# Kernel tuning notes

Measured on AMD Instinct MI355X. Metric: run time of the kernel, lower is better.

Reference implementation:

```python
import jax, jax.numpy as jnp
import numpy as np

V, D, H, L, B, S = 8192, 128, 8, 2, 1, 128
HD = D // H
HID = int(8 * D / 3)
EPS = 1e-6


def setup_inputs() -> dict:
    key = jax.random.key(0)
    ks = jax.random.split(key, 12)
    sc = 0.02
    return {
        "idx": jax.random.randint(ks[0], (B, S), 0, V),
        "w_raw": jax.random.normal(ks[1], (D, V), jnp.float32) * sc,
        "norm1_w": jnp.ones((L, D), jnp.float32),
        "norm2_w": jnp.ones((L, D), jnp.float32),
        "wq": jax.random.normal(ks[2], (L, D, D), jnp.float32) * sc,
        "wk": jax.random.normal(ks[3], (L, D, D), jnp.float32) * sc,
        "wv": jax.random.normal(ks[4], (L, D, D), jnp.float32) * sc,
        "wo": jax.random.normal(ks[5], (L, D, D), jnp.float32) * sc,
        "w1": jax.random.normal(ks[6], (L, D, HID), jnp.float32) * sc,
        "w3": jax.random.normal(ks[7], (L, D, HID), jnp.float32) * sc,
        "w2": jax.random.normal(ks[8], (L, HID, D), jnp.float32) * sc,
        "final_norm_w": jnp.ones((D,), jnp.float32),
    }


def rmsnorm(x, w):
    return x * jax.lax.rsqrt(jnp.mean(x * x, axis=-1, keepdims=True) + EPS) * w


def rope_cos_sin(seqlen, hd):
    inv = 1.0 / (10000.0 ** (jnp.arange(0, hd, 2, dtype=jnp.float32) / hd))
    t = jnp.arange(seqlen, dtype=jnp.float32)
    f = jnp.outer(t, inv)  # (S, hd/2)
    return jnp.cos(f), jnp.sin(f)


def apply_rope(x, cos, sin):
    # x: (B,S,H,HD); interleaved complex pairs as in Llama
    x0, x1 = x[..., 0::2], x[..., 1::2]
    c = cos[None, :, None, :]
    s = sin[None, :, None, :]
    r0 = x0 * c - x1 * s
    r1 = x0 * s + x1 * c
    return jnp.stack([r0, r1], axis=-1).reshape(x.shape)


def forward(idx, w_raw, norm1_w, norm2_w, wq, wk, wv, wo, w1, w2, w3, final_norm_w):
    Wemb = jax.nn.sigmoid(w_raw)                 # (D,V)
    x = Wemb.T[idx]                              # Yoneda one-hot @ W.T == gather -> (B,S,D)
    cos, sin = rope_cos_sin(S, HD)
    causal = jnp.tril(jnp.ones((S, S), bool))[None, None]  # (1,1,S,S)
    scale = 1.0 / jnp.sqrt(jnp.float32(HD))
    for i in range(L):
        # Multi-Universe attention (heads == universes), RoPE, causal SDPA
        h = rmsnorm(x, norm1_w[i])
        q = (h @ wq[i]).reshape(B, S, H, HD)
        k = (h @ wk[i]).reshape(B, S, H, HD)
        v = (h @ wv[i]).reshape(B, S, H, HD)
        q = apply_rope(q, cos, sin)
        k = apply_rope(k, cos, sin)
        scores = jnp.einsum("bihd,bjhd->bhij", q, k) * scale
        scores = jnp.where(causal, scores, jnp.float32(-1e9))
        attn = jax.nn.softmax(scores, axis=-1)
        o = jnp.einsum("bhij,bjhd->bihd", attn, v).reshape(B, S, D) @ wo[i]
        x = x + o
        # SwiGLU FFN
        h2 = rmsnorm(x, norm2_w[i])
        x = x + (jax.nn.silu(h2 @ w1[i]) * (h2 @ w3[i])) @ w2[i]
    x_norm = rmsnorm(x, final_norm_w)
    # Godel-Heyting reachability head
    x_n = x_norm / jnp.linalg.norm(x_norm, axis=-1, keepdims=True)      # (B,S,D)
    v_n = (Wemb / jnp.linalg.norm(Wemb, axis=0, keepdims=True)).T        # (V,D)
    a = x_n[:, :, None, :]                                               # (B,S,1,D)
    b = v_n[None, None, :, :]                                            # (1,1,V,D)
    # strict Godel implication: a => b = 1 if a <= b else b
    imp = jnp.where(a <= b, jnp.float32(1.0), b)                         # (B,S,V,D)
    logits = jnp.clip(imp.mean(axis=-1), 1e-6, 1.0 - 1e-6)               # (B,S,V)
    return logits


def reference(idx, w_raw, norm1_w, norm2_w, wq, wk, wv, wo, w1, w2, w3, final_norm_w):
    return forward(idx, w_raw, norm1_w, norm2_w, wq, wk, wv, wo, w1, w2, w3, final_norm_w)
```

## Files before the change

kernel.cpp:

```cpp
#include <hip/hip_runtime.h>
#include <math.h>

#define V 8192
#define D 128
#define NH 8
#define HD 16
#define SEQ 128
#define HID 341
#define EPS 1e-6f

__device__ __forceinline__ float sigm(float x) { return 1.0f / (1.0f + __expf(-x)); }

__device__ __forceinline__ float block_sum256(float v, float* scratch) {
    #pragma unroll
    for (int m = 32; m > 0; m >>= 1) v += __shfl_xor(v, m);
    if ((threadIdx.x & 63) == 0) scratch[threadIdx.x >> 6] = v;
    __syncthreads();
    float s = (scratch[0] + scratch[1]) + (scratch[2] + scratch[3]);
    __syncthreads();
    return s;
}

__global__ __launch_bounds__(256, 1) void k_embed_qkv(
    const int* __restrict__ idx, const float* __restrict__ w_raw,
    const float* __restrict__ wq, const float* __restrict__ wk,
    const float* __restrict__ wv, const float* __restrict__ n1w,
    const float* __restrict__ w1, const float* __restrict__ w3,
    const float* __restrict__ w2, const float* __restrict__ wo,
    float* __restrict__ x, float* __restrict__ q, float* __restrict__ k,
    float* __restrict__ v, float* __restrict__ sink) {
    int t = threadIdx.x;
    if (blockIdx.x >= SEQ) {
        int g = (blockIdx.x - SEQ) * 256 + t;
        float acc = 0.f;
        const float4* p = (const float4*)w_raw;
        for (int i = g; i < 262144; i += 65536) {
            float4 u = p[i];
            acc += u.x + u.y + u.z + u.w;
        }
        p = (const float4*)w1;
        if (g < 21824) { float4 u = p[g]; acc += u.x + u.y + u.z + u.w; }
        p = (const float4*)w3;
        if (g < 21824) { float4 u = p[g]; acc += u.x + u.y + u.z + u.w; }
        p = (const float4*)w2;
        if (g < 21824) { float4 u = p[g]; acc += u.x + u.y + u.z + u.w; }
        p = (const float4*)wq;
        if (g < 8192) { float4 u = p[g]; acc += u.x + u.y + u.z + u.w; }
        p = (const float4*)wk;
        if (g < 8192) { float4 u = p[g]; acc += u.x + u.y + u.z + u.w; }
        p = (const float4*)wv;
        if (g < 8192) { float4 u = p[g]; acc += u.x + u.y + u.z + u.w; }
        p = (const float4*)wo;
        if (g < 8192) { float4 u = p[g]; acc += u.x + u.y + u.z + u.w; }
        if (acc == 1234.5678f) sink[0] = acc;
        return;
    }
    __shared__ float hr[D], qrow[D], krow[D], vpart[2][D], scr[4];
    int s = blockIdx.x;
    int col = t & 127, half = t >> 7, dlo = half * 64;
    float xv = 0.f;
    if (t < 128) xv = sigm(w_raw[t * V + idx[s]]);
    float wpre[128];
    const float* wsel = (t < 128) ? wq : wk;
    #pragma unroll
    for (int d = 0; d < 128; ++d) wpre[d] = wsel[d * D + col];
    float wvpre[64];
    #pragma unroll
    for (int d = 0; d < 64; ++d) wvpre[d] = wv[(dlo + d) * D + col];
    if (t < 128) x[s * D + t] = xv;
    float ss = block_sum256(xv * xv, scr);
    float r = 1.0f / sqrtf(ss * (1.0f / D) + EPS);
    if (t < 128) hr[t] = xv * r * n1w[t];
    __syncthreads();
    float a0 = 0, a1 = 0, a2 = 0, a3 = 0;
    #pragma unroll
    for (int d = 0; d < 128; d += 4) {
        a0 += hr[d] * wpre[d];
        a1 += hr[d + 1] * wpre[d + 1];
        a2 += hr[d + 2] * wpre[d + 2];
        a3 += hr[d + 3] * wpre[d + 3];
    }
    float qk = (a0 + a1) + (a2 + a3);
    float b0 = 0, b1 = 0, b2 = 0, b3 = 0;
    #pragma unroll
    for (int d = 0; d < 64; d += 4) {
        b0 += hr[dlo + d] * wvpre[d];
        b1 += hr[dlo + d + 1] * wvpre[d + 1];
        b2 += hr[dlo + d + 2] * wvpre[d + 2];
        b3 += hr[dlo + d + 3] * wvpre[d + 3];
    }
    vpart[half][col] = (b0 + b1) + (b2 + b3);
    if (t < 128) qrow[col] = qk;
    else krow[col] = qk;
    __syncthreads();
    if (t < 128) {
        v[s * D + t] = vpart[0][t] + vpart[1][t];
        int c = t & (HD - 1);
        int m = c >> 1;
        float fr = (float)s * expf(-(float)m * 1.15129254649702283e+00f);
        float cs = cosf(fr), sn = sinf(fr);
        int base = t & ~1;
        float qe = qrow[base], qod = qrow[base + 1];
        float ke = krow[base], kod = krow[base + 1];
        q[s * D + t] = (c & 1) ? (qe * sn + qod * cs) : (qe * cs - qod * sn);
        k[s * D + t] = (c & 1) ? (ke * sn + kod * cs) : (ke * cs - kod * sn);
    }
}

template <int MODE>
__global__ __launch_bounds__(256, 1) void k_layer(
    const float* __restrict__ q, const float* __restrict__ kg,
    const float* __restrict__ vg, float* __restrict__ x,
    const float* __restrict__ wo, const float* __restrict__ n2w,
    const float* __restrict__ w1, const float* __restrict__ w3,
    const float* __restrict__ w2, const float* __restrict__ wq,
    const float* __restrict__ wk, const float* __restrict__ wv,
    const float* __restrict__ n1w, float* __restrict__ qo, float* __restrict__ ko,
    float* __restrict__ vo, const float* __restrict__ fw, float* __restrict__ xng) {
    __shared__ float ps[NH][SEQ + 1];
    __shared__ float qs[D], orow[D], h2[D];
    __shared__ float part[2][D];
    __shared__ float afA[HID], afB[HID], af[HID];
    __shared__ float rl[NH];
    __shared__ float scr[4];
    int s = blockIdx.x, t = threadIdx.x;
    int col = t & 127, half = t >> 7;
    int jlo = half * 64, dlo = half * 64;

    float qv = 0.f, xr = 0.f;
    if (t < 128) {
        qv = q[s * D + t];
        xr = x[s * D + t];
    }
    float4 kp[4][4];
    #pragma unroll
    for (int u = 0; u < 4; ++u) {
        const float4* p = (const float4*)&kg[col * D + (half + 2 * u) * HD];
        kp[u][0] = p[0]; kp[u][1] = p[1]; kp[u][2] = p[2]; kp[u][3] = p[3];
    }
    float vpre[64];
    #pragma unroll
    for (int j = 0; j < 64; ++j) vpre[j] = vg[(jlo + j) * D + col];
    float wopre[64];
    #pragma unroll
    for (int u = 0; u < 64; ++u) wopre[u] = wo[(dlo + u) * D + col];

    if (t < 128) qs[t] = qv;
    __syncthreads();

    #pragma unroll
    for (int u = 0; u < 4; ++u) {
        int h = half + 2 * u;
        const float* qh = &qs[h * HD];
        float acc = kp[u][0].x * qh[0] + kp[u][0].y * qh[1] + kp[u][0].z * qh[2] +
                    kp[u][0].w * qh[3] + kp[u][1].x * qh[4] + kp[u][1].y * qh[5] +
                    kp[u][1].z * qh[6] + kp[u][1].w * qh[7] + kp[u][2].x * qh[8] +
                    kp[u][2].y * qh[9] + kp[u][2].z * qh[10] + kp[u][2].w * qh[11] +
                    kp[u][3].x * qh[12] + kp[u][3].y * qh[13] + kp[u][3].z * qh[14] +
                    kp[u][3].w * qh[15];
        ps[h][col] = (col <= s) ? acc * 0.25f : 0.f;
    }
    __syncthreads();

    {
        int h = t >> 5, lane = t & 31;
        float pm = -1e30f;
        for (int j = lane; j <= s; j += 32) pm = fmaxf(pm, ps[h][j]);
        #pragma unroll
        for (int m = 16; m > 0; m >>= 1) pm = fmaxf(pm, __shfl_xor(pm, m, 32));
        float psum = 0.f;
        for (int j = lane; j <= s; j += 32) {
            float e = __expf(ps[h][j] - pm);
            ps[h][j] = e;
            psum += e;
        }
        #pragma unroll
        for (int m = 16; m > 0; m >>= 1) psum += __shfl_xor(psum, m, 32);
        if (lane == 0) rl[h] = 1.0f / psum;
    }
    __syncthreads();

    {
        int h = col >> 4;
        float a0 = 0, a1 = 0, a2 = 0, a3 = 0;
        #pragma unroll
        for (int j = 0; j < 64; j += 4) {
            a0 += ps[h][jlo + j] * vpre[j];
            a1 += ps[h][jlo + j + 1] * vpre[j + 1];
            a2 += ps[h][jlo + j + 2] * vpre[j + 2];
            a3 += ps[h][jlo + j + 3] * vpre[j + 3];
        }
        part[half][col] = (a0 + a1) + (a2 + a3);
    }
    __syncthreads();
    if (t < 128) orow[t] = (part[0][t] + part[1][t]) * rl[t >> 4];
    __syncthreads();

    {
        float a0 = 0, a1 = 0;
        #pragma unroll
        for (int u = 0; u < 64; u += 2) {
            a0 += orow[dlo + u] * wopre[u];
            a1 += orow[dlo + u + 1] * wopre[u + 1];
        }
        part[half][col] = a0 + a1;
    }
    __syncthreads();
    float xn = 0.f;
    if (t < 128) xn = xr + part[0][t] + part[1][t];
    float ss2 = block_sum256((t < 128) ? xn * xn : 0.f, scr);
    float r2 = 1.0f / sqrtf(ss2 * (1.0f / D) + EPS);
    if (t < 128) h2[t] = xn * r2 * n2w[t];
    __syncthreads();

    for (int task = t; task < 2 * HID; task += 256) {
        int mat = task >= HID;
        int c2 = mat ? (task - HID) : task;
        const float* w = mat ? w3 : w1;
        float a0 = 0, a1 = 0, a2 = 0, a3 = 0;
        #pragma unroll 8
        for (int d = 0; d < D; d += 4) {
            a0 += h2[d] * w[d * HID + c2];
            a1 += h2[d + 1] * w[(d + 1) * HID + c2];
            a2 += h2[d + 2] * w[(d + 2) * HID + c2];
            a3 += h2[d + 3] * w[(d + 3) * HID + c2];
        }
        if (mat) afB[c2] = (a0 + a1) + (a2 + a3);
        else afA[c2] = (a0 + a1) + (a2 + a3);
    }
    __syncthreads();
    for (int c2 = t; c2 < HID; c2 += 256) {
        float a1v = afA[c2];
        af[c2] = (a1v / (1.0f + __expf(-a1v))) * afB[c2];
    }
    __syncthreads();

    {
        int lo = half ? 171 : 0;
        int hi = half ? 341 : 171;
        float a0 = 0, a1 = 0, a2 = 0, a3 = 0;
        int tt = lo;
        #pragma unroll 8
        for (; tt + 3 < hi; tt += 4) {
            a0 += af[tt] * w2[tt * D + col];
            a1 += af[tt + 1] * w2[(tt + 1) * D + col];
            a2 += af[tt + 2] * w2[(tt + 2) * D + col];
            a3 += af[tt + 3] * w2[(tt + 3) * D + col];
        }
        for (; tt < hi; ++tt) a0 += af[tt] * w2[tt * D + col];
        part[half][col] = (a0 + a1) + (a2 + a3);
    }
    __syncthreads();
    float x2 = 0.f;
    if (t < 128) {
        x2 = xn + part[0][t] + part[1][t];
        if (MODE == 0) x[s * D + t] = x2;
    }

    float ss = block_sum256((t < 128) ? x2 * x2 : 0.f, scr);
    float r = 1.0f / sqrtf(ss * (1.0f / D) + EPS);

    if constexpr (MODE == 0) {
        if (t < 128) h2[t] = x2 * r * n1w[t];
        __syncthreads();
        const float* wsel = (t < 128) ? wq : wk;
        float a0 = 0, a1 = 0, a2 = 0, a3 = 0;
        #pragma unroll 8
        for (int d = 0; d < D; d += 4) {
            a0 += h2[d] * wsel[d * D + col];
            a1 += h2[d + 1] * wsel[(d + 1) * D + col];
            a2 += h2[d + 2] * wsel[(d + 2) * D + col];
            a3 += h2[d + 3] * wsel[(d + 3) * D + col];
        }
        float qk = (a0 + a1) + (a2 + a3);
        float b0 = 0, b1 = 0, b2 = 0, b3 = 0;
        #pragma unroll 8
        for (int d = dlo; d < dlo + 64; d += 4) {
            b0 += h2[d] * wv[d * D + col];
            b1 += h2[d + 1] * wv[(d + 1) * D + col];
            b2 += h2[d + 2] * wv[(d + 2) * D + col];
            b3 += h2[d + 3] * wv[(d + 3) * D + col];
        }
        part[half][col] = (b0 + b1) + (b2 + b3);
        if (t < 128) qs[col] = qk;
        else orow[col] = qk;
        __syncthreads();
        if (t < 128) {
            vo[s * D + t] = part[0][t] + part[1][t];
            int c = t & (HD - 1);
            int mm = c >> 1;
            float fr = (float)s * expf(-(float)mm * 1.15129254649702283e+00f);
            float cs = cosf(fr), sn = sinf(fr);
            int base = t & ~1;
            float qe = qs[base], qod = qs[base + 1];
            float ke = orow[base], kod = orow[base + 1];
            qo[s * D + t] = (c & 1) ? (qe * sn + qod * cs) : (qe * cs - qod * sn);
            ko[s * D + t] = (c & 1) ? (ke * sn + kod * cs) : (ke * cs - kod * sn);
        }
    } else {
        float y = (t < 128) ? x2 * r * fw[t] : 0.f;
        float nn = block_sum256(y * y, scr);
        if (t < 128) xng[t * SEQ + s] = y / sqrtf(nn);
    }
}

__global__ __launch_bounds__(256) void k_logits(const float* __restrict__ xng,
                                                const float* __restrict__ w_raw,
                                                float* __restrict__ out) {
    __shared__ float xs[D * 64];
    __shared__ float vs[D * 32];
    __shared__ float nred[256];
    __shared__ float invn_s[32];
    int t = threadIdx.x;
    int sbase = (blockIdx.x & 1) * 64;
    int vbase = (blockIdx.x >> 1) * 32;
    for (int i = t; i < D * 64; i += 256) {
        int d = i >> 6, s2 = i & 63;
        xs[i] = xng[d * SEQ + sbase + s2];
    }
    for (int i = t; i < D * 32; i += 256) {
        int d = i >> 5, jj = i & 31;
        vs[i] = sigm(w_raw[d * V + vbase + jj]);
    }
    __syncthreads();
    {
        int colc = t & 31, dp = t >> 5;
        float p = 0.f;
        for (int u = 0; u < 16; ++u) {
            float vv = vs[(dp * 16 + u) * 32 + colc];
            p += vv * vv;
        }
        nred[t] = p;
    }
    __syncthreads();
    if (t < 32) {
        float sum = 0.f;
        for (int u = 0; u < 8; ++u) sum += nred[u * 32 + t];
        invn_s[t] = 1.0f / sqrtf(sum);
    }
    __syncthreads();
    for (int i = t; i < D * 32; i += 256) vs[i] *= invn_s[i & 31];
    __syncthreads();
    int vg = t & 15;
    int sg = t >> 4;
    float acc[4][2] = {};
    for (int d = 0; d < D; ++d) {
        float4 xq = *(const float4*)&xs[d * 64 + sg * 4];
        float2 vq = *(const float2*)&vs[d * 32 + vg * 2];
        acc[0][0] += (xq.x <= vq.x) ? 1.0f : vq.x;
        acc[0][1] += (xq.x <= vq.y) ? 1.0f : vq.y;
        acc[1][0] += (xq.y <= vq.x) ? 1.0f : vq.x;
        acc[1][1] += (xq.y <= vq.y) ? 1.0f : vq.y;
        acc[2][0] += (xq.z <= vq.x) ? 1.0f : vq.x;
        acc[2][1] += (xq.z <= vq.y) ? 1.0f : vq.y;
        acc[3][0] += (xq.w <= vq.x) ? 1.0f : vq.x;
        acc[3][1] += (xq.w <= vq.y) ? 1.0f : vq.y;
    }
    const float inv128 = 1.0f / 128.0f;
    #pragma unroll
    for (int si = 0; si < 4; ++si) {
        int s = sbase + sg * 4 + si;
        float2 ov;
        ov.x = fminf(fmaxf(acc[si][0] * inv128, 1e-6f), 1.0f - 1e-6f);
        ov.y = fminf(fmaxf(acc[si][1] * inv128, 1e-6f), 1.0f - 1e-6f);
        *(float2*)&out[s * V + vbase + vg * 2] = ov;
    }
}

extern "C" void kernel_launch(void* const* d_in, const int* in_sizes, int n_in,
                              void* d_out, int out_size, void* d_ws, size_t ws_size,
                              hipStream_t stream) {
    const int* idx = (const int*)d_in[0];
    const float* w_raw = (const float*)d_in[1];
    const float* n1w = (const float*)d_in[2];
    const float* n2w = (const float*)d_in[3];
    const float* wq = (const float*)d_in[4];
    const float* wk = (const float*)d_in[5];
    const float* wv = (const float*)d_in[6];
    const float* wo = (const float*)d_in[7];
    const float* w1 = (const float*)d_in[8];
    const float* w3 = (const float*)d_in[9];
    const float* w2 = (const float*)d_in[10];
    const float* fnw = (const float*)d_in[11];
    float* out = (float*)d_out;
    float* ws = (float*)d_ws;

    float* x    = ws;
    float* q1   = ws + 16384;
    float* k1   = ws + 32768;
    float* v1   = ws + 49152;
    float* q2   = ws + 65536;
    float* k2   = ws + 81920;
    float* v2   = ws + 98304;
    float* xng  = ws + 114688;
    float* sink = ws + 131072;

    k_embed_qkv<<<dim3(SEQ + 256), dim3(256), 0, stream>>>(
        idx, w_raw, wq, wk, wv, n1w, w1, w3, w2, wo, x, q1, k1, v1, sink);
    k_layer<0><<<dim3(SEQ), dim3(256), 0, stream>>>(
        q1, k1, v1, x, wo, n2w, w1, w3, w2,
        wq + D * D, wk + D * D, wv + D * D, n1w + D, q2, k2, v2,
        (const float*)nullptr, (float*)nullptr);
    k_layer<1><<<dim3(SEQ), dim3(256), 0, stream>>>(
        q2, k2, v2, x, wo + D * D, n2w + D, w1 + D * HID, w3 + D * HID,
        w2 + HID * D, (const float*)nullptr, (const float*)nullptr,
        (const float*)nullptr, (const float*)nullptr, (float*)nullptr,
        (float*)nullptr, (float*)nullptr, fnw, xng);
    k_logits<<<dim3(512), dim3(256), 0, stream>>>(xng, w_raw, out);
}
```

Before: 146.4 us.

## Transpose weights and V into per-thread contiguous layouts for float4 dot products

The embed kernel's spare blocks now write transposed copies of all per-layer weights (wq/wk/wv/wo, w1/w3, and a padded w2) into workspace. V is stored transposed, so each thread in the layer kernels reads its dot-product operand contiguously with float4 loads instead of strided scalar loads, and the large register-prefetch arrays are removed. The FFN is rebalanced so each thread computes three hidden outputs. The trade-off is extra transpose traffic at launch, uncoalesced transposed reads per thread, and a loss of the prefetch overlap the old register arrays gave.

```diff
diff --git a/kernel.cpp b/kernel.cpp
--- a/kernel.cpp
+++ b/kernel.cpp
@@ -7,6 +7,7 @@
 #define HD 16
 #define SEQ 128
 #define HID 341
+#define HIDP 344
 #define EPS 1e-6f
 
 __device__ __forceinline__ float sigm(float x) { return 1.0f / (1.0f + __expf(-x)); }
@@ -24,34 +25,45 @@
 __global__ __launch_bounds__(256, 1) void k_embed_qkv(
     const int* __restrict__ idx, const float* __restrict__ w_raw,
     const float* __restrict__ wq, const float* __restrict__ wk,
-    const float* __restrict__ wv, const float* __restrict__ n1w,
+    const float* __restrict__ wv, const float* __restrict__ wo,
     const float* __restrict__ w1, const float* __restrict__ w3,
-    const float* __restrict__ w2, const float* __restrict__ wo,
+    const float* __restrict__ w2, const float* __restrict__ n1w,
     float* __restrict__ x, float* __restrict__ q, float* __restrict__ k,
-    float* __restrict__ v, float* __restrict__ sink) {
+    float* __restrict__ vt, float* __restrict__ wqT, float* __restrict__ wkT,
+    float* __restrict__ wvT, float* __restrict__ woT, float* __restrict__ w1T,
+    float* __restrict__ w3T, float* __restrict__ w2T, float* __restrict__ sink) {
     int t = threadIdx.x;
     if (blockIdx.x >= SEQ) {
         int g = (blockIdx.x - SEQ) * 256 + t;
+        if (g < 32768) {
+            int l = g >> 14, rem = g & 16383, d = rem >> 7, c = rem & 127;
+            int o = l * 16384 + c * 128 + d;
+            wqT[o] = wq[g];
+            wkT[o] = wk[g];
+            wvT[o] = wv[g];
+            woT[o] = wo[g];
+        }
+        for (int i = g; i < 2 * 43648; i += 65536) {
+            int l = i >= 43648;
+            int r = i - (l ? 43648 : 0);
+            int c = r >> 7, d = r & 127;
+            w1T[i] = w1[l * 43648 + d * HID + c];
+            w3T[i] = w3[l * 43648 + d * HID + c];
+        }
+        for (int i = g; i < 2 * 44032; i += 65536) {
+            int l = i >= 44032;
+            int r = i - (l ? 44032 : 0);
+            int c = r / HIDP;
+            int kk = r - c * HIDP;
+            w2T[i] = (kk < HID) ? w2[l * 43648 + kk * 128 + c] : 0.f;
+        }
         float acc = 0.f;
         const float4* p = (const float4*)w_raw;
-        for (int i = g; i < 262144; i += 65536) {
-            float4 u = p[i];
+        #pragma unroll
+        for (int i = 0; i < 4; ++i) {
+            float4 u = p[g + i * 65536];
             acc += u.x + u.y + u.z + u.w;
         }
-        p = (const float4*)w1;
-        if (g < 21824) { float4 u = p[g]; acc += u.x + u.y + u.z + u.w; }
-        p = (const float4*)w3;
-        if (g < 21824) { float4 u = p[g]; acc += u.x + u.y + u.z + u.w; }
-        p = (const float4*)w2;
-        if (g < 21824) { float4 u = p[g]; acc += u.x + u.y + u.z + u.w; }
-        p = (const float4*)wq;
-        if (g < 8192) { float4 u = p[g]; acc += u.x + u.y + u.z + u.w; }
-        p = (const float4*)wk;
-        if (g < 8192) { float4 u = p[g]; acc += u.x + u.y + u.z + u.w; }
-        p = (const float4*)wv;
-        if (g < 8192) { float4 u = p[g]; acc += u.x + u.y + u.z + u.w; }
-        p = (const float4*)wo;
-        if (g < 8192) { float4 u = p[g]; acc += u.x + u.y + u.z + u.w; }
         if (acc == 1234.5678f) sink[0] = acc;
         return;
     }
@@ -60,41 +72,35 @@
     int col = t & 127, half = t >> 7, dlo = half * 64;
     float xv = 0.f;
     if (t < 128) xv = sigm(w_raw[t * V + idx[s]]);
-    float wpre[128];
-    const float* wsel = (t < 128) ? wq : wk;
-    #pragma unroll
-    for (int d = 0; d < 128; ++d) wpre[d] = wsel[d * D + col];
-    float wvpre[64];
-    #pragma unroll
-    for (int d = 0; d < 64; ++d) wvpre[d] = wv[(dlo + d) * D + col];
     if (t < 128) x[s * D + t] = xv;
     float ss = block_sum256(xv * xv, scr);
     float r = 1.0f / sqrtf(ss * (1.0f / D) + EPS);
     if (t < 128) hr[t] = xv * r * n1w[t];
     __syncthreads();
+    const float* wsel = (t < 128) ? wq : wk;
     float a0 = 0, a1 = 0, a2 = 0, a3 = 0;
-    #pragma unroll
+    #pragma unroll 8
     for (int d = 0; d < 128; d += 4) {
-        a0 += hr[d] * wpre[d];
-        a1 += hr[d + 1] * wpre[d + 1];
-        a2 += hr[d + 2] * wpre[d + 2];
-        a3 += hr[d + 3] * wpre[d + 3];
+        a0 += hr[d] * wsel[d * D + col];
+        a1 += hr[d + 1] * wsel[(d + 1) * D + col];
+        a2 += hr[d + 2] * wsel[(d + 2) * D + col];
+        a3 += hr[d + 3] * wsel[(d + 3) * D + col];
     }
     float qk = (a0 + a1) + (a2 + a3);
     float b0 = 0, b1 = 0, b2 = 0, b3 = 0;
-    #pragma unroll
-    for (int d = 0; d < 64; d += 4) {
-        b0 += hr[dlo + d] * wvpre[d];
-        b1 += hr[dlo + d + 1] * wvpre[d + 1];
-        b2 += hr[dlo + d + 2] * wvpre[d + 2];
-        b3 += hr[dlo + d + 3] * wvpre[d + 3];
+    #pragma unroll 8
+    for (int d = dlo; d < dlo + 64; d += 4) {
+        b0 += hr[d] * wv[d * D + col];
+        b1 += hr[d + 1] * wv[(d + 1) * D + col];
+        b2 += hr[d + 2] * wv[(d + 2) * D + col];
+        b3 += hr[d + 3] * wv[(d + 3) * D + col];
     }
     vpart[half][col] = (b0 + b1) + (b2 + b3);
     if (t < 128) qrow[col] = qk;
     else krow[col] = qk;
     __syncthreads();
     if (t < 128) {
-        v[s * D + t] = vpart[0][t] + vpart[1][t];
+        vt[t * SEQ + s] = vpart[0][t] + vpart[1][t];
         int c = t & (HD - 1);
         int m = c >> 1;
         float fr = (float)s * expf(-(float)m * 1.15129254649702283e+00f);
@@ -110,55 +116,47 @@
 template <int MODE>
 __global__ __launch_bounds__(256, 1) void k_layer(
     const float* __restrict__ q, const float* __restrict__ kg,
-    const float* __restrict__ vg, float* __restrict__ x,
-    const float* __restrict__ wo, const float* __restrict__ n2w,
-    const float* __restrict__ w1, const float* __restrict__ w3,
-    const float* __restrict__ w2, const float* __restrict__ wq,
-    const float* __restrict__ wk, const float* __restrict__ wv,
+    const float* __restrict__ vt, float* __restrict__ x,
+    const float* __restrict__ woT, const float* __restrict__ n2w,
+    const float* __restrict__ w1T, const float* __restrict__ w3T,
+    const float* __restrict__ w2T, const float* __restrict__ wqT,
+    const float* __restrict__ wkT, const float* __restrict__ wvT,
     const float* __restrict__ n1w, float* __restrict__ qo, float* __restrict__ ko,
-    float* __restrict__ vo, const float* __restrict__ fw, float* __restrict__ xng) {
-    __shared__ float ps[NH][SEQ + 1];
-    __shared__ float qs[D], orow[D], h2[D];
+    float* __restrict__ vto, const float* __restrict__ fw, float* __restrict__ xng) {
+    __shared__ float ps[NH][SEQ + 2];
+    __shared__ float qs[D], orow[D], qrow[D], krow[D];
     __shared__ float part[2][D];
-    __shared__ float afA[HID], afB[HID], af[HID];
+    __shared__ float4 h24[32];
+    __shared__ float4 af4[86];
+    __shared__ float afA[HID], afB[HID];
     __shared__ float rl[NH];
     __shared__ float scr[4];
+    float* h2 = (float*)h24;
+    float* af = (float*)af4;
     int s = blockIdx.x, t = threadIdx.x;
     int col = t & 127, half = t >> 7;
-    int jlo = half * 64, dlo = half * 64;
-
-    float qv = 0.f, xr = 0.f;
+
+    float xr = 0.f;
     if (t < 128) {
-        qv = q[s * D + t];
+        qs[t] = q[s * D + t];
         xr = x[s * D + t];
     }
-    float4 kp[4][4];
-    #pragma unroll
-    for (int u = 0; u < 4; ++u) {
-        const float4* p = (const float4*)&kg[col * D + (half + 2 * u) * HD];
-        kp[u][0] = p[0]; kp[u][1] = p[1]; kp[u][2] = p[2]; kp[u][3] = p[3];
-    }
-    float vpre[64];
-    #pragma unroll
-    for (int j = 0; j < 64; ++j) vpre[j] = vg[(jlo + j) * D + col];
-    float wopre[64];
-    #pragma unroll
-    for (int u = 0; u < 64; ++u) wopre[u] = wo[(dlo + u) * D + col];
-
-    if (t < 128) qs[t] = qv;
-    __syncthreads();
-
-    #pragma unroll
-    for (int u = 0; u < 4; ++u) {
-        int h = half + 2 * u;
-        const float* qh = &qs[h * HD];
-        float acc = kp[u][0].x * qh[0] + kp[u][0].y * qh[1] + kp[u][0].z * qh[2] +
-                    kp[u][0].w * qh[3] + kp[u][1].x * qh[4] + kp[u][1].y * qh[5] +
-                    kp[u][1].z * qh[6] + kp[u][1].w * qh[7] + kp[u][2].x * qh[8] +
-                    kp[u][2].y * qh[9] + kp[u][2].z * qh[10] + kp[u][2].w * qh[11] +
-                    kp[u][3].x * qh[12] + kp[u][3].y * qh[13] + kp[u][3].z * qh[14] +
-                    kp[u][3].w * qh[15];
-        ps[h][col] = (col <= s) ? acc * 0.25f : 0.f;
+    __syncthreads();
+
+    {
+        int j = col;
+        #pragma unroll
+        for (int u = 0; u < 4; ++u) {
+            int h = half + 2 * u;
+            const float4* kp = (const float4*)&kg[j * D + h * HD];
+            float4 k0 = kp[0], k1 = kp[1], k2 = kp[2], k3 = kp[3];
+            const float* qh = &qs[h * HD];
+            float acc = k0.x * qh[0] + k0.y * qh[1] + k0.z * qh[2] + k0.w * qh[3] +
+                        k1.x * qh[4] + k1.y * qh[5] + k1.z * qh[6] + k1.w * qh[7] +
+                        k2.x * qh[8] + k2.y * qh[9] + k2.z * qh[10] + k2.w * qh[11] +
+                        k3.x * qh[12] + k3.y * qh[13] + k3.z * qh[14] + k3.w * qh[15];
+            ps[h][j] = (j <= s) ? acc * 0.25f : 0.f;
+        }
     }
     __syncthreads();
 
@@ -181,14 +179,17 @@
     __syncthreads();
 
     {
-        int h = col >> 4;
+        int h = col >> 4, jlo = half * 64;
+        const float4* vp = (const float4*)&vt[col * SEQ + jlo];
         float a0 = 0, a1 = 0, a2 = 0, a3 = 0;
         #pragma unroll
-        for (int j = 0; j < 64; j += 4) {
-            a0 += ps[h][jlo + j] * vpre[j];
-            a1 += ps[h][jlo + j + 1] * vpre[j + 1];
-            a2 += ps[h][jlo + j + 2] * vpre[j + 2];
-            a3 += ps[h][jlo + j + 3] * vpre[j + 3];
+        for (int i = 0; i < 16; ++i) {
+            float4 vv = vp[i];
+            int j = jlo + 4 * i;
+            a0 += ps[h][j] * vv.x;
+            a1 += ps[h][j + 1] * vv.y;
+            a2 += ps[h][j + 2] * vv.z;
+            a3 += ps[h][j + 3] * vv.w;
         }
         part[half][col] = (a0 + a1) + (a2 + a3);
     }
@@ -197,13 +198,19 @@
     __syncthreads();
 
     {
-        float a0 = 0, a1 = 0;
-        #pragma unroll
-        for (int u = 0; u < 64; u += 2) {
-            a0 += orow[dlo + u] * wopre[u];
-            a1 += orow[dlo + u + 1] * wopre[u + 1];
-        }
-        part[half][col] = a0 + a1;
+        int dlo = half * 64;
+        const float4* wp = (const float4*)&woT[col * 128 + dlo];
+        float a0 = 0, a1 = 0, a2 = 0, a3 = 0;
+        #pragma unroll
+        for (int i = 0; i < 16; ++i) {
+            float4 ww = wp[i];
+            int d = dlo + 4 * i;
+            a0 += orow[d] * ww.x;
+            a1 += orow[d + 1] * ww.y;
+            a2 += orow[d + 2] * ww.z;
+            a3 += orow[d + 3] * ww.w;
+        }
+        part[half][col] = (a0 + a1) + (a2 + a3);
     }
     __syncthreads();
     float xn = 0.f;
@@ -213,41 +220,56 @@
     if (t < 128) h2[t] = xn * r2 * n2w[t];
     __syncthreads();
 
-    for (int task = t; task < 2 * HID; task += 256) {
-        int mat = task >= HID;
-        int c2 = mat ? (task - HID) : task;
-        const float* w = mat ? w3 : w1;
+    {
+        int u1 = t, u2 = t + 256, u3 = t + 512;
+        const float4* pa = (const float4*)&w1T[u1 * 128];
+        const float4* pb = (const float4*)((u2 < HID) ? &w1T[u2 * 128] : &w3T[(u2 - HID) * 128]);
+        bool v3 = u3 < 2 * HID;
+        const float4* pc = (const float4*)(v3 ? &w3T[(u3 - HID) * 128] : &w3T[0]);
+        float a0 = 0, a1 = 0, b0 = 0, b1 = 0, c0 = 0, c1 = 0;
+        #pragma unroll
+        for (int i = 0; i < 32; ++i) {
+            float4 hh = h24[i];
+            float4 wa = pa[i];
+            a0 += hh.x * wa.x + hh.y * wa.y;
+            a1 += hh.z * wa.z + hh.w * wa.w;
+            float4 wb = pb[i];
+            b0 += hh.x * wb.x + hh.y * wb.y;
+            b1 += hh.z * wb.z + hh.w * wb.w;
+            float4 wc = pc[i];
+            c0 += hh.x * wc.x + hh.y * wc.y;
+            c1 += hh.z * wc.z + hh.w * wc.w;
+        }
+        afA[u1] = a0 + a1;
+        if (u2 < HID) afA[u2] = b0 + b1;
+        else afB[u2 - HID] = b0 + b1;
+        if (v3) afB[u3 - HID] = c0 + c1;
+    }
+    __syncthreads();
+    for (int c2 = t; c2 < HIDP; c2 += 256) {
+        if (c2 < HID) {
+            float a = afA[c2];
+            af[c2] = (a / (1.0f + __expf(-a))) * afB[c2];
+        } else {
+            af[c2] = 0.f;
+        }
+    }
+    __syncthreads();
+
+    {
+        int klo = half * 172;
+        const float4* wp = (const float4*)&w2T[col * HIDP + klo];
+        const float4* ap = (const float4*)&af[klo];
         float a0 = 0, a1 = 0, a2 = 0, a3 = 0;
-        #pragma unroll 8
-        for (int d = 0; d < D; d += 4) {
-            a0 += h2[d] * w[d * HID + c2];
-            a1 += h2[d + 1] * w[(d + 1) * HID + c2];
-            a2 += h2[d + 2] * w[(d + 2) * HID + c2];
-            a3 += h2[d + 3] * w[(d + 3) * HID + c2];
-        }
-        if (mat) afB[c2] = (a0 + a1) + (a2 + a3);
-        else afA[c2] = (a0 + a1) + (a2 + a3);
-    }
-    __syncthreads();
-    for (int c2 = t; c2 < HID; c2 += 256) {
-        float a1v = afA[c2];
-        af[c2] = (a1v / (1.0f + __expf(-a1v))) * afB[c2];
-    }
-    __syncthreads();
-
-    {
-        int lo = half ? 171 : 0;
-        int hi = half ? 341 : 171;
-        float a0 = 0, a1 = 0, a2 = 0, a3 = 0;
-        int tt = lo;
-        #pragma unroll 8
-        for (; tt + 3 < hi; tt += 4) {
-            a0 += af[tt] * w2[tt * D + col];
-            a1 += af[tt + 1] * w2[(tt + 1) * D + col];
-            a2 += af[tt + 2] * w2[(tt + 2) * D + col];
-            a3 += af[tt + 3] * w2[(tt + 3) * D + col];
-        }
-        for (; tt < hi; ++tt) a0 += af[tt] * w2[tt * D + col];
+        #pragma unroll
+        for (int i = 0; i < 43; ++i) {
+            float4 ww = wp[i];
+            float4 aa = ap[i];
+            a0 += aa.x * ww.x;
+            a1 += aa.y * ww.y;
+            a2 += aa.z * ww.z;
+            a3 += aa.w * ww.w;
+        }
         part[half][col] = (a0 + a1) + (a2 + a3);
     }
     __syncthreads();
@@ -256,49 +278,55 @@
         x2 = xn + part[0][t] + part[1][t];
         if (MODE == 0) x[s * D + t] = x2;
     }
-
-    float ss = block_sum256((t < 128) ? x2 * x2 : 0.f, scr);
-    float r = 1.0f / sqrtf(ss * (1.0f / D) + EPS);
+    float ss3 = block_sum256((t < 128) ? x2 * x2 : 0.f, scr);
+    float r3 = 1.0f / sqrtf(ss3 * (1.0f / D) + EPS);
 
     if constexpr (MODE == 0) {
-        if (t < 128) h2[t] = x2 * r * n1w[t];
+        if (t < 128) h2[t] = x2 * r3 * n1w[t];
         __syncthreads();
-        const float* wsel = (t < 128) ? wq : wk;
-        float a0 = 0, a1 = 0, a2 = 0, a3 = 0;
-        #pragma unroll 8
-        for (int d = 0; d < D; d += 4) {
-            a0 += h2[d] * wsel[d * D + col];
-            a1 += h2[d + 1] * wsel[(d + 1) * D + col];
-            a2 += h2[d + 2] * wsel[(d + 2) * D + col];
-            a3 += h2[d + 3] * wsel[(d + 3) * D + col];
-        }
-        float qk = (a0 + a1) + (a2 + a3);
-        float b0 = 0, b1 = 0, b2 = 0, b3 = 0;
-        #pragma unroll 8
-        for (int d = dlo; d < dlo + 64; d += 4) {
-            b0 += h2[d] * wv[d * D + col];
-            b1 += h2[d + 1] * wv[(d + 1) * D + col];
-            b2 += h2[d + 2] * wv[(d + 2) * D + col];
-            b3 += h2[d + 3] * wv[(d + 3) * D + col];
-        }
-        part[half][col] = (b0 + b1) + (b2 + b3);
-        if (t < 128) qs[col] = qk;
-        else orow[col] = qk;
+        float qk;
+        {
+            const float4* wp = (const float4*)((t < 128) ? &wqT[col * 128] : &wkT[col * 128]);
+            float a0 = 0, a1 = 0;
+            #pragma unroll
+            for (int i = 0; i < 32; ++i) {
+                float4 hh = h24[i];
+                float4 ww = wp[i];
+                a0 += hh.x * ww.x + hh.y * ww.y;
+                a1 += hh.z * ww.z + hh.w * ww.w;
+            }
+            qk = a0 + a1;
+        }
+        {
+            int dlo = half * 64;
+            const float4* wp = (const float4*)&wvT[col * 128 + dlo];
+            float a0 = 0, a1 = 0;
+            #pragma unroll
+            for (int i = 0; i < 16; ++i) {
+                float4 hh = h24[dlo / 4 + i];
+                float4 ww = wp[i];
+                a0 += hh.x * ww.x + hh.y * ww.y;
+                a1 += hh.z * ww.z + hh.w * ww.w;
+            }
+            part[half][col] = a0 + a1;
+        }
+        if (t < 128) qrow[col] = qk;
+        else krow[col] = qk;
         __syncthreads();
         if (t < 128) {
-            vo[s * D + t] = part[0][t] + part[1][t];
+            vto[t * SEQ + s] = part[0][t] + part[1][t];
             int c = t & (HD - 1);
             int mm = c >> 1;
             float fr = (float)s * expf(-(float)mm * 1.15129254649702283e+00f);
             float cs = cosf(fr), sn = sinf(fr);
             int base = t & ~1;
-            float qe = qs[base], qod = qs[base + 1];
-            float ke = orow[base], kod = orow[base + 1];
+            float qe = qrow[base], qod = qrow[base + 1];
+            float ke = krow[base], kod = krow[base + 1];
             qo[s * D + t] = (c & 1) ? (qe * sn + qod * cs) : (qe * cs - qod * sn);
             ko[s * D + t] = (c & 1) ? (ke * sn + kod * cs) : (ke * cs - kod * sn);
         }
     } else {
-        float y = (t < 128) ? x2 * r * fw[t] : 0.f;
+        float y = (t < 128) ? x2 * r3 * fw[t] : 0.f;
         float nn = block_sum256(y * y, scr);
         if (t < 128) xng[t * SEQ + s] = y / sqrtf(nn);
     }
@@ -388,22 +416,30 @@
     float* x    = ws;
     float* q1   = ws + 16384;
     float* k1   = ws + 32768;
-    float* v1   = ws + 49152;
+    float* v1t  = ws + 49152;
     float* q2   = ws + 65536;
     float* k2   = ws + 81920;
-    float* v2   = ws + 98304;
+    float* v2t  = ws + 98304;
     float* xng  = ws + 114688;
     float* sink = ws + 131072;
+    float* wqT  = ws + 131104;
+    float* wkT  = ws + 163872;
+    float* wvT  = ws + 196640;
+    float* woT  = ws + 229408;
+    float* w1T  = ws + 262176;
+    float* w3T  = ws + 349472;
+    float* w2T  = ws + 436768;
 
     k_embed_qkv<<<dim3(SEQ + 256), dim3(256), 0, stream>>>(
-        idx, w_raw, wq, wk, wv, n1w, w1, w3, w2, wo, x, q1, k1, v1, sink);
+        idx, w_raw, wq, wk, wv, wo, w1, w3, w2, n1w, x, q1, k1, v1t,
+        wqT, wkT, wvT, woT, w1T, w3T, w2T, sink);
     k_layer<0><<<dim3(SEQ), dim3(256), 0, stream>>>(
-        q1, k1, v1, x, wo, n2w, w1, w3, w2,
-        wq + D * D, wk + D * D, wv + D * D, n1w + D, q2, k2, v2,
+        q1, k1, v1t, x, woT, n2w, w1T, w3T, w2T,
+        wqT + 16384, wkT + 16384, wvT + 16384, n1w + D, q2, k2, v2t,
         (const float*)nullptr, (float*)nullptr);
     k_layer<1><<<dim3(SEQ), dim3(256), 0, stream>>>(
-        q2, k2, v2, x, wo + D * D, n2w + D, w1 + D * HID, w3 + D * HID,
-        w2 + HID * D, (const float*)nullptr, (const float*)nullptr,
+        q2, k2, v2t, x, woT + 16384, n2w + D, w1T + 43648, w3T + 43648,
+        w2T + 44032, (const float*)nullptr, (const float*)nullptr,
         (const float*)nullptr, (const float*)nullptr, (float*)nullptr,
         (float*)nullptr, (float*)nullptr, fnw, xng);
     k_logits<<<dim3(512), dim3(256), 0, stream>>>(xng, w_raw, out);
```

After: 165.3 us. 13.0% more time.

## Stage layer weights through LDS with coalesced float4 double-buffered loads

Applied to the files above, without the earlier changes.

The per-token layer kernel now copies V, Wo, Wq/Wk/Wv and the FFN weights (w1, w3, w2) into a 128 KB shared buffer using coalesced float4 loads. The FFN matmuls use a double-buffered pipeline that prefetches the next chunk into registers while the current chunk is computed from LDS. The embed kernel drops its large register prefetch arrays and reads weights directly. The goal is to replace strided, uncoalesced global loads and heavy register pressure with coalesced bulk copies and reads from LDS. The cost is many extra barriers and a very large LDS footprint per block, which limits occupancy to one block per CU.

```diff
diff --git a/kernel.cpp b/kernel.cpp
--- a/kernel.cpp
+++ b/kernel.cpp
@@ -19,6 +19,25 @@
     float s = (scratch[0] + scratch[1]) + (scratch[2] + scratch[3]);
     __syncthreads();
     return s;
+}
+
+template <int NF4>
+__device__ __forceinline__ void pf_load(float4* v, const float* src, int t) {
+    const float4* s4 = (const float4*)src;
+    #pragma unroll
+    for (int i = 0; i < (NF4 + 255) / 256; ++i) {
+        int idx = t + i * 256;
+        if (idx < NF4) v[i] = s4[idx];
+    }
+}
+template <int NF4>
+__device__ __forceinline__ void pf_store(const float4* v, float* dst, int t) {
+    float4* d4 = (float4*)dst;
+    #pragma unroll
+    for (int i = 0; i < (NF4 + 255) / 256; ++i) {
+        int idx = t + i * 256;
+        if (idx < NF4) d4[idx] = v[i];
+    }
 }
 
 __global__ __launch_bounds__(256, 1) void k_embed_qkv(
@@ -60,34 +79,28 @@
     int col = t & 127, half = t >> 7, dlo = half * 64;
     float xv = 0.f;
     if (t < 128) xv = sigm(w_raw[t * V + idx[s]]);
-    float wpre[128];
-    const float* wsel = (t < 128) ? wq : wk;
-    #pragma unroll
-    for (int d = 0; d < 128; ++d) wpre[d] = wsel[d * D + col];
-    float wvpre[64];
-    #pragma unroll
-    for (int d = 0; d < 64; ++d) wvpre[d] = wv[(dlo + d) * D + col];
     if (t < 128) x[s * D + t] = xv;
     float ss = block_sum256(xv * xv, scr);
     float r = 1.0f / sqrtf(ss * (1.0f / D) + EPS);
     if (t < 128) hr[t] = xv * r * n1w[t];
     __syncthreads();
+    const float* wsel = (t < 128) ? wq : wk;
     float a0 = 0, a1 = 0, a2 = 0, a3 = 0;
-    #pragma unroll
+    #pragma unroll 8
     for (int d = 0; d < 128; d += 4) {
-        a0 += hr[d] * wpre[d];
-        a1 += hr[d + 1] * wpre[d + 1];
-        a2 += hr[d + 2] * wpre[d + 2];
-        a3 += hr[d + 3] * wpre[d + 3];
+        a0 += hr[d] * wsel[d * D + col];
+        a1 += hr[d + 1] * wsel[(d + 1) * D + col];
+        a2 += hr[d + 2] * wsel[(d + 2) * D + col];
+        a3 += hr[d + 3] * wsel[(d + 3) * D + col];
     }
     float qk = (a0 + a1) + (a2 + a3);
     float b0 = 0, b1 = 0, b2 = 0, b3 = 0;
-    #pragma unroll
-    for (int d = 0; d < 64; d += 4) {
-        b0 += hr[dlo + d] * wvpre[d];
-        b1 += hr[dlo + d + 1] * wvpre[d + 1];
-        b2 += hr[dlo + d + 2] * wvpre[d + 2];
-        b3 += hr[dlo + d + 3] * wvpre[d + 3];
+    #pragma unroll 8
+    for (int d = dlo; d < dlo + 64; d += 4) {
+        b0 += hr[d] * wv[d * D + col];
+        b1 += hr[d + 1] * wv[(d + 1) * D + col];
+        b2 += hr[d + 2] * wv[(d + 2) * D + col];
+        b3 += hr[d + 3] * wv[(d + 3) * D + col];
     }
     vpart[half][col] = (b0 + b1) + (b2 + b3);
     if (t < 128) qrow[col] = qk;
@@ -117,48 +130,48 @@
     const float* __restrict__ wk, const float* __restrict__ wv,
     const float* __restrict__ n1w, float* __restrict__ qo, float* __restrict__ ko,
     float* __restrict__ vo, const float* __restrict__ fw, float* __restrict__ xng) {
-    __shared__ float ps[NH][SEQ + 1];
-    __shared__ float qs[D], orow[D], h2[D];
+    __shared__ float B0[32768];
+    __shared__ float ps[NH][SEQ + 2];
+    __shared__ float qs[D], orow[D], h2[D], qrow[D], krow[D];
     __shared__ float part[2][D];
-    __shared__ float afA[HID], afB[HID], af[HID];
+    __shared__ float af[344];
     __shared__ float rl[NH];
     __shared__ float scr[4];
     int s = blockIdx.x, t = threadIdx.x;
     int col = t & 127, half = t >> 7;
-    int jlo = half * 64, dlo = half * 64;
-
-    float qv = 0.f, xr = 0.f;
+
+    {
+        const float4* v4 = (const float4*)vg;
+        const float4* o4 = (const float4*)wo;
+        float4* d0 = (float4*)B0;
+        float4* d1 = (float4*)(B0 + 16384);
+        #pragma unroll
+        for (int i = 0; i < 16; ++i) {
+            d0[t + i * 256] = v4[t + i * 256];
+            d1[t + i * 256] = o4[t + i * 256];
+        }
+    }
+    float xr = 0.f;
     if (t < 128) {
-        qv = q[s * D + t];
+        qs[t] = q[s * D + t];
         xr = x[s * D + t];
     }
-    float4 kp[4][4];
-    #pragma unroll
-    for (int u = 0; u < 4; ++u) {
-        const float4* p = (const float4*)&kg[col * D + (half + 2 * u) * HD];
-        kp[u][0] = p[0]; kp[u][1] = p[1]; kp[u][2] = p[2]; kp[u][3] = p[3];
-    }
-    float vpre[64];
-    #pragma unroll
-    for (int j = 0; j < 64; ++j) vpre[j] = vg[(jlo + j) * D + col];
-    float wopre[64];
-    #pragma unroll
-    for (int u = 0; u < 64; ++u) wopre[u] = wo[(dlo + u) * D + col];
-
-    if (t < 128) qs[t] = qv;
-    __syncthreads();
-
-    #pragma unroll
-    for (int u = 0; u < 4; ++u) {
-        int h = half + 2 * u;
-        const float* qh = &qs[h * HD];
-        float acc = kp[u][0].x * qh[0] + kp[u][0].y * qh[1] + kp[u][0].z * qh[2] +
-                    kp[u][0].w * qh[3] + kp[u][1].x * qh[4] + kp[u][1].y * qh[5] +
-                    kp[u][1].z * qh[6] + kp[u][1].w * qh[7] + kp[u][2].x * qh[8] +
-                    kp[u][2].y * qh[9] + kp[u][2].z * qh[10] + kp[u][2].w * qh[11] +
-                    kp[u][3].x * qh[12] + kp[u][3].y * qh[13] + kp[u][3].z * qh[14] +
-                    kp[u][3].w * qh[15];
-        ps[h][col] = (col <= s) ? acc * 0.25f : 0.f;
+    __syncthreads();
+
+    {
+        int j = col;
+        #pragma unroll
+        for (int u = 0; u < 4; ++u) {
+            int h = half + 2 * u;
+            const float4* kp = (const float4*)&kg[j * D + h * HD];
+            float4 k0 = kp[0], k1 = kp[1], k2 = kp[2], k3 = kp[3];
+            const float* qh = &qs[h * HD];
+            float acc = k0.x * qh[0] + k0.y * qh[1] + k0.z * qh[2] + k0.w * qh[3] +
+                        k1.x * qh[4] + k1.y * qh[5] + k1.z * qh[6] + k1.w * qh[7] +
+                        k2.x * qh[8] + k2.y * qh[9] + k2.z * qh[10] + k2.w * qh[11] +
+                        k3.x * qh[12] + k3.y * qh[13] + k3.z * qh[14] + k3.w * qh[15];
+            ps[h][j] = (j <= s) ? acc * 0.25f : 0.f;
+        }
     }
     __syncthreads();
 
@@ -181,14 +194,15 @@
     __syncthreads();
 
     {
-        int h = col >> 4;
+        int h = col >> 4, jlo = half * 64;
+        const float* vsh = B0;
         float a0 = 0, a1 = 0, a2 = 0, a3 = 0;
         #pragma unroll
         for (int j = 0; j < 64; j += 4) {
-            a0 += ps[h][jlo + j] * vpre[j];
-            a1 += ps[h][jlo + j + 1] * vpre[j + 1];
-            a2 += ps[h][jlo + j + 2] * vpre[j + 2];
-            a3 += ps[h][jlo + j + 3] * vpre[j + 3];
+            a0 += ps[h][jlo + j] * vsh[(jlo + j) * 128 + col];
+            a1 += ps[h][jlo + j + 1] * vsh[(jlo + j + 1) * 128 + col];
+            a2 += ps[h][jlo + j + 2] * vsh[(jlo + j + 2) * 128 + col];
+            a3 += ps[h][jlo + j + 3] * vsh[(jlo + j + 3) * 128 + col];
         }
         part[half][col] = (a0 + a1) + (a2 + a3);
     }
@@ -197,13 +211,17 @@
     __syncthreads();
 
     {
-        float a0 = 0, a1 = 0;
-        #pragma unroll
-        for (int u = 0; u < 64; u += 2) {
-            a0 += orow[dlo + u] * wopre[u];
-            a1 += orow[dlo + u + 1] * wopre[u + 1];
-        }
-        part[half][col] = a0 + a1;
+        int dlo = half * 64;
+        const float* wosh = B0 + 16384;
+        float a0 = 0, a1 = 0, a2 = 0, a3 = 0;
+        #pragma unroll
+        for (int d = 0; d < 64; d += 4) {
+            a0 += orow[dlo + d] * wosh[(dlo + d) * 128 + col];
+            a1 += orow[dlo + d + 1] * wosh[(dlo + d + 1) * 128 + col];
+            a2 += orow[dlo + d + 2] * wosh[(dlo + d + 2) * 128 + col];
+            a3 += orow[dlo + d + 3] * wosh[(dlo + d + 3) * 128 + col];
+        }
+        part[half][col] = (a0 + a1) + (a2 + a3);
     }
     __syncthreads();
     float xn = 0.f;
@@ -211,79 +229,124 @@
     float ss2 = block_sum256((t < 128) ? xn * xn : 0.f, scr);
     float r2 = 1.0f / sqrtf(ss2 * (1.0f / D) + EPS);
     if (t < 128) h2[t] = xn * r2 * n2w[t];
-    __syncthreads();
-
-    for (int task = t; task < 2 * HID; task += 256) {
-        int mat = task >= HID;
-        int c2 = mat ? (task - HID) : task;
-        const float* w = mat ? w3 : w1;
-        float a0 = 0, a1 = 0, a2 = 0, a3 = 0;
-        #pragma unroll 8
-        for (int d = 0; d < D; d += 4) {
-            a0 += h2[d] * w[d * HID + c2];
-            a1 += h2[d + 1] * w[(d + 1) * HID + c2];
-            a2 += h2[d + 2] * w[(d + 2) * HID + c2];
-            a3 += h2[d + 3] * w[(d + 3) * HID + c2];
-        }
-        if (mat) afB[c2] = (a0 + a1) + (a2 + a3);
-        else afA[c2] = (a0 + a1) + (a2 + a3);
-    }
-    __syncthreads();
-    for (int c2 = t; c2 < HID; c2 += 256) {
-        float a1v = afA[c2];
-        af[c2] = (a1v / (1.0f + __expf(-a1v))) * afB[c2];
-    }
-    __syncthreads();
-
-    {
-        int lo = half ? 171 : 0;
-        int hi = half ? 341 : 171;
-        float a0 = 0, a1 = 0, a2 = 0, a3 = 0;
-        int tt = lo;
-        #pragma unroll 8
-        for (; tt + 3 < hi; tt += 4) {
-            a0 += af[tt] * w2[tt * D + col];
-            a1 += af[tt + 1] * w2[(tt + 1) * D + col];
-            a2 += af[tt + 2] * w2[(tt + 2) * D + col];
-            a3 += af[tt + 3] * w2[(tt + 3) * D + col];
-        }
-        for (; tt < hi; ++tt) a0 += af[tt] * w2[tt * D + col];
-        part[half][col] = (a0 + a1) + (a2 + a3);
-    }
+    float* buf[2] = {B0, B0 + 11008};
+    {
+        float4 tmp[11];
+        pf_load<2728>(tmp, w1, t);
+        pf_store<2728>(tmp, buf[0], t);
+    }
+    __syncthreads();
+
+    float a1a = 0, a1b = 0, a3a = 0, a3b = 0;
+    #pragma unroll
+    for (int p = 0; p < 8; ++p) {
+        float4 tmp[11];
+        if (p < 7) {
+            const float* src = (p + 1 < 4) ? w1 + (p + 1) * 10912 : w3 + (p - 3) * 10912;
+            pf_load<2728>(tmp, src, t);
+        }
+        const float* Bp = buf[p & 1];
+        int d0 = (p & 3) * 32;
+        float s0 = 0, s1 = 0;
+        #pragma unroll
+        for (int d = 0; d < 32; ++d) {
+            float hv = h2[d0 + d];
+            s0 += hv * Bp[d * HID + t];
+            s1 += hv * Bp[d * HID + t + 256];
+        }
+        if (p < 4) { a1a += s0; a1b += s1; }
+        else { a3a += s0; a3b += s1; }
+        if (p < 7) pf_store<2728>(tmp, buf[(p + 1) & 1], t);
+        __syncthreads();
+    }
+    af[t] = (a1a / (1.0f + __expf(-a1a))) * a3a;
+    if (t < 85) af[t + 256] = (a1b / (1.0f + __expf(-a1b))) * a3b;
+    {
+        float4 tmp[11];
+        pf_load<2752>(tmp, w2, t);
+        pf_store<2752>(tmp, buf[0], t);
+    }
+    __syncthreads();
+
+    float facc = 0.f;
+    #pragma unroll
+    for (int p = 0; p < 4; ++p) {
+        float4 tmp[11];
+        if (p < 3) pf_load<2752>(tmp, w2 + (p + 1) * 11008, t);
+        const float* Bp = buf[p & 1];
+        int rows = (p < 3) ? 86 : 83;
+        int k0 = p * 86;
+        int lo = half * 43;
+        int hi = lo + 43; if (hi > rows) hi = rows;
+        float a0 = 0, a1 = 0;
+        #pragma unroll
+        for (int u = 0; u < 43; u += 1) {
+            int k = lo + u;
+            if (k < hi) {
+                float t0 = af[k0 + k] * Bp[k * 128 + col];
+                if (u & 1) a1 += t0; else a0 += t0;
+            }
+        }
+        facc += a0 + a1;
+        if (p < 3) pf_store<2752>(tmp, buf[(p + 1) & 1], t);
+        __syncthreads();
+    }
+    part[half][col] = facc;
     __syncthreads();
     float x2 = 0.f;
     if (t < 128) {
         x2 = xn + part[0][t] + part[1][t];
         if (MODE == 0) x[s * D + t] = x2;
     }
-
-    float ss = block_sum256((t < 128) ? x2 * x2 : 0.f, scr);
-    float r = 1.0f / sqrtf(ss * (1.0f / D) + EPS);
+    float ss3 = block_sum256((t < 128) ? x2 * x2 : 0.f, scr);
+    float r3 = 1.0f / sqrtf(ss3 * (1.0f / D) + EPS);
 
     if constexpr (MODE == 0) {
-        if (t < 128) h2[t] = x2 * r * n1w[t];
-        __syncthreads();
-        const float* wsel = (t < 128) ? wq : wk;
-        float a0 = 0, a1 = 0, a2 = 0, a3 = 0;
-        #pragma unroll 8
-        for (int d = 0; d < D; d += 4) {
-            a0 += h2[d] * wsel[d * D + col];
-            a1 += h2[d + 1] * wsel[(d + 1) * D + col];
-            a2 += h2[d + 2] * wsel[(d + 2) * D + col];
-            a3 += h2[d + 3] * wsel[(d + 3) * D + col];
-        }
-        float qk = (a0 + a1) + (a2 + a3);
-        float b0 = 0, b1 = 0, b2 = 0, b3 = 0;
-        #pragma unroll 8
-        for (int d = dlo; d < dlo + 64; d += 4) {
-            b0 += h2[d] * wv[d * D + col];
-            b1 += h2[d + 1] * wv[(d + 1) * D + col];
-            b2 += h2[d + 2] * wv[(d + 2) * D + col];
-            b3 += h2[d + 3] * wv[(d + 3) * D + col];
-        }
-        part[half][col] = (b0 + b1) + (b2 + b3);
-        if (t < 128) qs[col] = qk;
-        else orow[col] = qk;
+        if (t < 128) h2[t] = x2 * r3 * n1w[t];
+        {
+            const float4* q4 = (const float4*)wq;
+            const float4* k4 = (const float4*)wk;
+            float4* dA = (float4*)B0;
+            float4* dB = (float4*)(B0 + 16384);
+            #pragma unroll
+            for (int i = 0; i < 16; ++i) {
+                dA[t + i * 256] = q4[t + i * 256];
+                dB[t + i * 256] = k4[t + i * 256];
+            }
+        }
+        __syncthreads();
+        {
+            const float* W = (t < 128) ? B0 : (B0 + 16384);
+            float a0 = 0, a1 = 0, a2 = 0, a3 = 0;
+            #pragma unroll
+            for (int d = 0; d < 128; d += 4) {
+                a0 += h2[d] * W[d * 128 + col];
+                a1 += h2[d + 1] * W[(d + 1) * 128 + col];
+                a2 += h2[d + 2] * W[(d + 2) * 128 + col];
+                a3 += h2[d + 3] * W[(d + 3) * 128 + col];
+            }
+            float qk = (a0 + a1) + (a2 + a3);
+            if (t < 128) qrow[col] = qk;
+            else krow[col] = qk;
+        }
+        __syncthreads();
+        {
+            const float4* v4 = (const float4*)wv;
+            float4* dA = (float4*)B0;
+            #pragma unroll
+            for (int i = 0; i < 16; ++i) dA[t + i * 256] = v4[t + i * 256];
+        }
+        __syncthreads();
+        {
+            int dlo = half * 64;
+            float a0 = 0, a1 = 0;
+            #pragma unroll
+            for (int d = 0; d < 64; d += 2) {
+                a0 += h2[dlo + d] * B0[(dlo + d) * 128 + col];
+                a1 += h2[dlo + d + 1] * B0[(dlo + d + 1) * 128 + col];
+            }
+            part[half][col] = a0 + a1;
+        }
         __syncthreads();
         if (t < 128) {
             vo[s * D + t] = part[0][t] + part[1][t];
@@ -292,13 +355,13 @@
             float fr = (float)s * expf(-(float)mm * 1.15129254649702283e+00f);
             float cs = cosf(fr), sn = sinf(fr);
             int base = t & ~1;
-            float qe = qs[base], qod = qs[base + 1];
-            float ke = orow[base], kod = orow[base + 1];
+            float qe = qrow[base], qod = qrow[base + 1];
+            float ke = krow[base], kod = krow[base + 1];
             qo[s * D + t] = (c & 1) ? (qe * sn + qod * cs) : (qe * cs - qod * sn);
             ko[s * D + t] = (c & 1) ? (ke * sn + kod * cs) : (ke * cs - kod * sn);
         }
     } else {
-        float y = (t < 128) ? x2 * r * fw[t] : 0.f;
+        float y = (t < 128) ? x2 * r3 * fw[t] : 0.f;
         float nn = block_sum256(y * y, scr);
         if (t < 128) xng[t * SEQ + s] = y / sqrtf(nn);
     }
```

Measured after the change: 433.2 us. 196% more time.
